# Kernel optimization log

Hardware: AMD Instinct MI355X
Metric: run time of the kernel (lower is better)

## Reference

```python
import jax, jax.numpy as jnp
import numpy as np
from jax import lax

B0, H0, W0, C0 = 16, 32, 32, 512
D_ = C0 // 4      # per-group channels = d_inner (expand=1)
S = 1             # d_state
R = 8             # dt_rank = ceil(D_/16)


def layernorm(x, w, b, eps=1e-5):
    m = jnp.mean(x, axis=-1, keepdims=True)
    v = jnp.mean((x - m) ** 2, axis=-1, keepdims=True)
    return (x - m) / jnp.sqrt(v + eps) * w + b


def silu(x):
    return x * jax.nn.sigmoid(x)


def selective_scan(u, delta, A, Bs, Cs, Dp):
    # u,delta:(B,d,L)  A:(d,S)  Bs,Cs:(B,S,L)  Dp:(d,)
    a = jnp.exp(jnp.einsum('bdl,ds->bdsl', delta, A))      # decay per step
    bx = jnp.einsum('bdl,bsl,bdl->bdsl', delta, Bs, u)     # input injection
    def comb(c1, c2):
        a1, b1 = c1
        a2, b2 = c2
        return (a1 * a2, a2 * b1 + b2)
    _, h = lax.associative_scan(comb, (a, bx), axis=-1)    # h_t = a_t h_{t-1} + b_t
    return jnp.einsum('bdsl,bsl->bdl', h, Cs) + Dp[None, :, None] * u


def ss2d(xg, direction, ipw, cw, cb, xpw, dtw, dtb, Alog, Dp, onw, onb, opw):
    # xg: (B,H,W,dm); single-direction SS2D branch (CrossScan_i / CrossMerge_i)
    Bsz, Hh, Ww, dm = xg.shape
    xz = jnp.einsum('bhwc,oc->bhwo', xg, ipw)              # in_proj -> 2*d_inner
    xc, z = jnp.split(xz, 2, axis=-1)
    xc = xc.transpose(0, 3, 1, 2)                           # (B,d,H,W)
    xc = lax.conv_general_dilated(xc, cw, (1, 1), [(1, 1), (1, 1)],
                                  dimension_numbers=('NCHW', 'OIHW', 'NCHW'),
                                  feature_group_count=dm) + cb[None, :, None, None]
    xc = silu(xc)
    L = Hh * Ww
    if direction == 0:
        xs = xc.reshape(Bsz, dm, L)                         # row-major forward
    elif direction == 1:
        xs = xc.transpose(0, 1, 3, 2).reshape(Bsz, dm, L)   # column-major forward
    elif direction == 2:
        xs = xc.reshape(Bsz, dm, L)[:, :, ::-1]             # row-major reversed
    else:
        xs = xc.transpose(0, 1, 3, 2).reshape(Bsz, dm, L)[:, :, ::-1]
    xd = jnp.einsum('bdl,cd->bcl', xs, xpw)                 # x_proj -> (dt,B,C)
    dts, Bc, Cc = jnp.split(xd, [R, R + S], axis=1)
    delta = jax.nn.softplus(jnp.einsum('brl,dr->bdl', dts, dtw) + dtb[None, :, None])
    A = -jnp.exp(Alog)                                      # (d,S)
    y = selective_scan(xs, delta, A, Bc, Cc, Dp)
    if direction == 0:
        yhw = y.reshape(Bsz, dm, Hh, Ww)
    elif direction == 1:
        yhw = y.reshape(Bsz, dm, Ww, Hh).transpose(0, 1, 3, 2)
    elif direction == 2:
        yhw = y[:, :, ::-1].reshape(Bsz, dm, Hh, Ww)
    else:
        yhw = y[:, :, ::-1].reshape(Bsz, dm, Ww, Hh).transpose(0, 1, 3, 2)
    yo = yhw.transpose(0, 2, 3, 1)                          # (B,H,W,d)
    yo = layernorm(yo, onw, onb)
    yo = yo * silu(z)
    return jnp.einsum('bhwd,od->bhwo', yo, opw)             # out_proj


def setup_inputs() -> dict:
    key = jax.random.key(0)
    ks = jax.random.split(key, 12)
    def rn(k, shape, scale=0.02):
        return (jax.random.normal(k, shape) * scale).astype(jnp.float32)
    return dict(
        x=jax.random.normal(ks[0], (B0, H0 * W0, C0), dtype=jnp.float32),
        H=H0, W=W0,
        norm_w=jnp.ones((C0,), jnp.float32), norm_b=jnp.zeros((C0,), jnp.float32),
        fc_w=rn(ks[1], (C0, C0)), fc_b=jnp.zeros((C0,), jnp.float32),
        eca_w=rn(ks[2], (3,), 0.3),
        skip_scale=jnp.ones((), jnp.float32),
        proj_w=rn(ks[3], (C0, C0)), proj_b=jnp.zeros((C0,), jnp.float32),
        in_proj_w=rn(ks[4], (4, 2 * D_, D_)),
        conv_w=rn(ks[5], (4, D_, 1, 3, 3), 0.1), conv_b=jnp.zeros((4, D_), jnp.float32),
        x_proj_w=rn(ks[6], (4, R + 2 * S, D_)),
        dt_proj_w=rn(ks[7], (4, D_, R), 0.1), dt_proj_b=rn(ks[8], (4, D_), 0.1),
        A_log=jnp.zeros((4, D_, S), jnp.float32),           # A = -1 (d_state=1 init)
        D_param=jnp.ones((4, D_), jnp.float32),
        out_norm_w=jnp.ones((4, D_), jnp.float32), out_norm_b=jnp.zeros((4, D_), jnp.float32),
        out_proj_w=rn(ks[9], (4, D_, D_)),
    )


def reference(x, H, W, norm_w, norm_b, fc_w, fc_b, eca_w, skip_scale, proj_w, proj_b,
              in_proj_w, conv_w, conv_b, x_proj_w, dt_proj_w, dt_proj_b, A_log, D_param,
              out_norm_w, out_norm_b, out_proj_w):
    Bsz, N, Cc = x.shape
    xn = layernorm(x, norm_w, norm_b)
    # ECA-style channel gate: mean over tokens, 1D conv (k=3) over channel axis
    z_avg = jnp.mean(xn, axis=1)                            # (B,C)
    zp = jnp.pad(z_avg, ((0, 0), (1, 1)))
    y_eca = eca_w[0] * zp[:, :-2] + eca_w[1] * zp[:, 1:-1] + eca_w[2] * zp[:, 2:]
    gate = jax.nn.sigmoid(jnp.einsum('bc,oc->bo', z_avg, fc_w) + fc_b + y_eca)
    xh = xn.reshape(Bsz, H, W, Cc)
    groups = jnp.split(xh, 4, axis=-1)
    ys = []
    for g in range(4):                                      # 4 directional SS2D branches
        ys.append(ss2d(groups[g], g, in_proj_w[g], conv_w[g], conv_b[g], x_proj_w[g],
                       dt_proj_w[g], dt_proj_b[g], A_log[g], D_param[g],
                       out_norm_w[g], out_norm_b[g], out_proj_w[g]))
    xm = jnp.concatenate(ys, axis=-1) * skip_scale * xh
    xm = xm.reshape(Bsz, N, Cc) * gate[:, None, :]
    xm = layernorm(xm, norm_w, norm_b)
    return jnp.einsum('bnc,oc->bno', xm, proj_w) + proj_b
```

## Files before the change

### kernel.cpp

```cpp
#include <hip/hip_runtime.h>
#include <math.h>

#define NTOK 16384
#define NC 512
#define ND 128
#define NCH 64
#define CST 16

typedef __attribute__((ext_vector_type(8))) short bf16x8;
typedef __attribute__((ext_vector_type(4))) float f32x4;

#define LOG2E 1.4426950408889634f
#define LN2   0.6931471805599453f

__device__ __forceinline__ float fexp(float x){ return __builtin_amdgcn_exp2f(x * LOG2E); }
__device__ __forceinline__ float flog(float x){ return __builtin_amdgcn_logf(x) * LN2; }
__device__ __forceinline__ float sigf(float x){ return 1.f/(1.f + fexp(-x)); }

__device__ __forceinline__ float b2f(ushort u){ unsigned x = ((unsigned)u)<<16; return __builtin_bit_cast(float,x); }
__device__ __forceinline__ ushort f2b(float f){
  unsigned u = __builtin_bit_cast(unsigned,f);
  u += 0x7fff + ((u>>16)&1);
  return (ushort)(u>>16);
}

__device__ __forceinline__ int perm_pos(int g, int l){
  switch(g){
    case 0: return l;
    case 1: return ((l & 31) << 5) | (l >> 5);
    case 2: return 1023 - l;
    default:{ int ll = 1023 - l; return ((ll & 31) << 5) | (ll >> 5); }
  }
}

__device__ __forceinline__ void gload16(const void* g, void* l){
  __builtin_amdgcn_global_load_lds((const __attribute__((address_space(1))) void*)g,
                                   (__attribute__((address_space(3))) void*)l, 16, 0, 0);
}

__global__ __launch_bounds__(256) void k_tobf16_4(
    const float* __restrict__ s1, int n1, ushort* __restrict__ d1,
    const float* __restrict__ s2, int n2, ushort* __restrict__ d2,
    const float* __restrict__ s3, int n3, ushort* __restrict__ d3,
    const float* __restrict__ s4, int n4, ushort* __restrict__ d4){
  int i = blockIdx.x*256 + threadIdx.x;
  if (i < n1) d1[i] = f2b(s1[i]);
  else if (i < n1+n2) d2[i-n1] = f2b(s2[i-n1]);
  else if (i < n1+n2+n3) d3[i-n1-n2] = f2b(s3[i-n1-n2]);
  else if (i < n1+n2+n3+n4) d4[i-n1-n2-n3] = f2b(s4[i-n1-n2-n3]);
}

__global__ __launch_bounds__(256) void k_ln512(const float* __restrict__ x,
    const float* __restrict__ w, const float* __restrict__ b, ushort* __restrict__ out){
  int wv = threadIdx.x >> 6, lane = threadIdx.x & 63;
  int t = blockIdx.x*4 + wv;
  const float* xr = x + (size_t)t*NC + lane*8;
  float4 a = *(const float4*)xr;
  float4 c = *(const float4*)(xr+4);
  float e[8] = {a.x,a.y,a.z,a.w,c.x,c.y,c.z,c.w};
  float s = 0.f, sq = 0.f;
  #pragma unroll
  for (int i=0;i<8;i++){ s += e[i]; sq += e[i]*e[i]; }
  #pragma unroll
  for (int o=1;o<64;o<<=1){ s += __shfl_xor(s,o); sq += __shfl_xor(sq,o); }
  float m = s*(1.f/NC);
  float var = sq*(1.f/NC) - m*m;
  float rs = rsqrtf(var + 1e-5f);
  const float4* wr = (const float4*)(w + lane*8);
  const float4* br = (const float4*)(b + lane*8);
  float4 w0 = wr[0], w1 = wr[1], b0 = br[0], b1 = br[1];
  float wv8[8] = {w0.x,w0.y,w0.z,w0.w,w1.x,w1.y,w1.z,w1.w};
  float bv8[8] = {b0.x,b0.y,b0.z,b0.w,b1.x,b1.y,b1.z,b1.w};
  bf16x8 o8;
  #pragma unroll
  for (int i=0;i<8;i++) ((ushort*)&o8)[i] = f2b((e[i]-m)*rs*wv8[i]+bv8[i]);
  *(bf16x8*)(out + (size_t)t*NC + lane*8) = o8;
}

__global__ __launch_bounds__(512) void k_cm1(const ushort* __restrict__ xn,
    float* __restrict__ part){
  int c = threadIdx.x;
  const ushort* base = xn + ((size_t)blockIdx.x*32)*NC + c;
  float acc = 0.f;
  for (int n=0;n<32;n++) acc += b2f(base[(size_t)n*NC]);
  part[(size_t)blockIdx.x*NC + c] = acc;
}
__global__ __launch_bounds__(512) void k_cm2(const float* __restrict__ part,
    float* __restrict__ zavg){
  int b = blockIdx.x, c = threadIdx.x;
  float acc = 0.f;
  for (int i=0;i<32;i++) acc += part[(size_t)(b*32+i)*NC + c];
  zavg[b*NC+c] = acc * (1.f/1024.f);
}

__global__ __launch_bounds__(256) void k_gate(const float* __restrict__ zavg,
    const float* __restrict__ fcw, const float* __restrict__ fcb,
    const float* __restrict__ ew, float* __restrict__ gate){
  __shared__ float za[NC];
  int b = blockIdx.x >> 7, og = blockIdx.x & 127;
  int tid = threadIdx.x, lane = tid & 63, wv = tid >> 6;
  za[tid]     = zavg[b*NC + tid];
  za[tid+256] = zavg[b*NC + tid + 256];
  __syncthreads();
  int o = og*4 + wv;
  const float* wr = fcw + (size_t)o*NC;
  float acc = 0.f;
  #pragma unroll
  for (int i=0;i<8;i++) acc += za[lane + i*64]*wr[lane + i*64];
  #pragma unroll
  for (int off=1;off<64;off<<=1) acc += __shfl_xor(acc, off);
  if (lane==0){
    float left  = (o>0)    ? za[o-1] : 0.f;
    float right = (o<NC-1) ? za[o+1] : 0.f;
    float ye = ew[0]*left + ew[1]*za[o] + ew[2]*right;
    gate[b*NC+o] = sigf(acc + fcb[o] + ye);
  }
}

__global__ __launch_bounds__(256) void k_gemm_bf16(
    const ushort* __restrict__ A, int lda, long sAz,
    const ushort* __restrict__ Bw, int ldb, long sBz, int K,
    ushort* __restrict__ C0, int ldc0, ushort* __restrict__ C1, int ldc1,
    int nsplit, long sCz,
    float* __restrict__ Cf, int ldcf, const float* __restrict__ bias)
{
  __shared__ __align__(16) ushort Asm[128*64];
  __shared__ __align__(16) ushort Bsm[128*64];
  const int z = blockIdx.z;
  A  += (size_t)z*sAz;
  Bw += (size_t)z*sBz;
  if (C0) C0 += (size_t)z*sCz;
  if (C1) C1 += (size_t)z*sCz;
  const int tid = threadIdx.x;
  const int lane = tid & 63, wid = tid >> 6;
  const int wm = wid >> 1, wn = wid & 1;
  const int m0 = blockIdx.y * 128, n0 = blockIdx.x * 128;

  const ushort* ga[4]; const ushort* gb[4]; int ldst[4];
  #pragma unroll
  for (int j=0;j<4;j++){
    int c = tid + 256*j;
    int r = c >> 3;
    int kb = ((c & 7) << 4) ^ ((r & 7) << 4);
    ga[j] = A  + (size_t)(m0 + r)*lda + (kb >> 1);
    gb[j] = Bw + (size_t)(n0 + r)*ldb + (kb >> 1);
    ldst[j] = c * 8;
  }

  f32x4 acc[4][4];
  #pragma unroll
  for (int i=0;i<4;i++)
    #pragma unroll
    for (int j=0;j<4;j++) acc[i][j] = (f32x4){0.f,0.f,0.f,0.f};

  const int lc = lane & 15;
  const int kgrp = (lane >> 4) << 4;

  for (int k0 = 0; k0 < K; k0 += 64){
    #pragma unroll
    for (int j=0;j<4;j++) gload16(ga[j] + k0, Asm + ldst[j]);
    #pragma unroll
    for (int j=0;j<4;j++) gload16(gb[j] + k0, Bsm + ldst[j]);
    __syncthreads();
    #pragma unroll
    for (int kk=0; kk<2; kk++){
      bf16x8 af[4], bfr[4];
      #pragma unroll
      for (int i=0;i<4;i++){
        int ra = wm*64 + i*16 + lc;
        int kb = kk*64 + kgrp;
        af[i] = *(const bf16x8*)((const char*)Asm + ra*128 + (kb ^ ((ra&7)<<4)));
        int rb = wn*64 + i*16 + lc;
        bfr[i] = *(const bf16x8*)((const char*)Bsm + rb*128 + (kb ^ ((rb&7)<<4)));
      }
      #pragma unroll
      for (int i=0;i<4;i++)
        #pragma unroll
        for (int j=0;j<4;j++)
          acc[i][j] = __builtin_amdgcn_mfma_f32_16x16x32_bf16(af[i], bfr[j], acc[i][j], 0, 0, 0);
    }
    __syncthreads();
  }

  const int lr = (lane >> 4) * 4;
  if (Cf){
    #pragma unroll
    for (int i=0;i<4;i++)
      #pragma unroll
      for (int j=0;j<4;j++){
        int row = m0 + wm*64 + i*16 + lr;
        int col = n0 + wn*64 + j*16 + lc;
        float bv = bias ? bias[col] : 0.f;
        #pragma unroll
        for (int r=0;r<4;r++)
          Cf[(size_t)(row+r)*ldcf + col] = acc[i][j][r] + bv;
      }
  } else {
    #pragma unroll
    for (int i=0;i<4;i++)
      #pragma unroll
      for (int j=0;j<4;j++){
        int row = m0 + wm*64 + i*16 + lr;
        int col = n0 + wn*64 + j*16 + lc;
        #pragma unroll
        for (int r=0;r<4;r++){
          ushort hv = f2b(acc[i][j][r]);
          if (col < nsplit) C0[(size_t)(row+r)*ldc0 + col] = hv;
          else              C1[(size_t)(row+r)*ldc1 + col - nsplit] = hv;
        }
      }
  }
}

__global__ __launch_bounds__(256) void k_convxp(const ushort* __restrict__ xc,
    const float* __restrict__ cw, const float* __restrict__ cb,
    const ushort* __restrict__ xpw_b, ushort* __restrict__ u, float* __restrict__ xd){
  __shared__ __align__(16) ushort xin[4*32*128];
  __shared__ __align__(16) ushort su[64][136];
  int g = blockIdx.z, tid = threadIdx.x;
  int blk = blockIdx.x;
  int bimg = blk >> 4, rp = blk & 15;
  int t0 = blk * 64;
  const ushort* xcg = xc + (size_t)g*NTOK*ND;

  #pragma unroll
  for (int j=0;j<8;j++){
    int c = tid + 256*j;
    int r = c >> 9;
    int rest = c & 511;
    int gr = 2*rp + r - 1;
    gr = min(max(gr, 0), 31);
    int w = rest >> 4, p = rest & 15;
    gload16(xcg + ((size_t)((bimg<<10) | (gr<<5) | w))*ND + p*8, (ushort*)xin + c*8);
  }

  int p = tid & 15, d0 = p*8;
  float w_[9][8]; float bias[8];
  {
    const float* wk = cw + (size_t)(g*ND + d0)*9;
    #pragma unroll
    for (int j=0;j<8;j++)
      #pragma unroll
      for (int k9=0;k9<9;k9++) w_[k9][j] = wk[j*9+k9];
    const float* cbp = cb + g*ND + d0;
    #pragma unroll
    for (int j=0;j<8;j++) bias[j] = cbp[j];
  }
  __syncthreads();

  #pragma unroll
  for (int pass=0; pass<4; pass++){
    int lt = pass*16 + (tid>>4);
    int hl = lt >> 5, w = lt & 31;
    int t = t0 + lt;
    float acc[8];
    #pragma unroll
    for (int j=0;j<8;j++) acc[j] = bias[j];
    #pragma unroll
    for (int kh=0;kh<3;kh++){
      int gr = 2*rp + hl + kh - 1;
      if (gr < 0 || gr >= 32) continue;
      #pragma unroll
      for (int kw=0;kw<3;kw++){
        int w2 = w + kw - 1;
        if (w2 < 0 || w2 >= 32) continue;
        bf16x8 v = *(const bf16x8*)&xin[((hl+kh)*32 + w2)*128 + d0];
        #pragma unroll
        for (int j=0;j<8;j++) acc[j] = fmaf(b2f(((ushort*)&v)[j]), w_[kh*3+kw][j], acc[j]);
      }
    }
    bf16x8 o8;
    #pragma unroll
    for (int j=0;j<8;j++){
      float uv = acc[j] * sigf(acc[j]);
      ((ushort*)&o8)[j] = f2b(uv);
    }
    *(bf16x8*)(u + ((size_t)g*NTOK + t)*ND + d0) = o8;
    *(bf16x8*)&su[lt][d0] = o8;
  }
  __syncthreads();

  int lane = tid & 63, wv = tid >> 6;
  int c = lane & 15;
  int kg = (lane >> 4) * 8;
  int cc = c < 10 ? c : 0;
  f32x4 acc4 = (f32x4){0.f,0.f,0.f,0.f};
  #pragma unroll
  for (int ks=0; ks<4; ks++){
    bf16x8 af = *(const bf16x8*)&su[wv*16 + (lane & 15)][ks*32 + kg];
    bf16x8 bfv = *(const bf16x8*)(xpw_b + (size_t)(g*10+cc)*128 + ks*32 + kg);
    if (c >= 10) bfv = (bf16x8){0,0,0,0,0,0,0,0};
    acc4 = __builtin_amdgcn_mfma_f32_16x16x32_bf16(af, bfv, acc4, 0, 0, 0);
  }
  if (c < 10){
    #pragma unroll
    for (int r=0;r<4;r++){
      int row = (lane >> 4)*4 + r;
      int t = t0 + wv*16 + row;
      xd[((size_t)g*NTOK + t)*12 + c] = acc4[r];
    }
  }
}

struct ScanCtx {
  float Ad, dtb_d;
  float w[8];
};

__device__ __forceinline__ void scan_step(const ScanCtx& c, float uv,
    const float4& x0, const float4& x1, float Bv,
    float& h, float& ap){
  float a = c.dtb_d;
  a = fmaf(x0.x, c.w[0], a); a = fmaf(x0.y, c.w[1], a);
  a = fmaf(x0.z, c.w[2], a); a = fmaf(x0.w, c.w[3], a);
  a = fmaf(x1.x, c.w[4], a); a = fmaf(x1.y, c.w[5], a);
  a = fmaf(x1.z, c.w[6], a); a = fmaf(x1.w, c.w[7], a);
  float dl = (a > 15.f) ? a : flog(1.f + fexp(a));
  float av = fexp(dl * c.Ad);
  h = fmaf(av, h, dl*Bv*uv);
  ap *= av;
}

__global__ __launch_bounds__(128) void k_scan1(const ushort* __restrict__ u,
    const float* __restrict__ xd, const float* __restrict__ Alog,
    const float* __restrict__ dtw, const float* __restrict__ dtb,
    float* __restrict__ chA, float* __restrict__ chB){
  int d = threadIdx.x, g = blockIdx.z;
  int b = blockIdx.x >> 6, ch = blockIdx.x & 63;
  ScanCtx c;
  c.Ad = -fexp(Alog[g*ND+d]);
  c.dtb_d = dtb[g*ND+d];
  const float4* wr = (const float4*)(dtw + (size_t)(g*ND+d)*8);
  float4 w0 = wr[0], w1 = wr[1];
  c.w[0]=w0.x;c.w[1]=w0.y;c.w[2]=w0.z;c.w[3]=w0.w;
  c.w[4]=w1.x;c.w[5]=w1.y;c.w[6]=w1.z;c.w[7]=w1.w;
  float h = 0.f, ap = 1.f;
  int l0 = ch*CST;
  #pragma unroll 4
  for (int s=0;s<CST;s++){
    int pp = perm_pos(g, l0 + s);
    size_t base = (size_t)g*NTOK + ((b<<10)|pp);
    float uv = b2f(u[base*ND + d]);
    const float4* xr = (const float4*)(xd + base*12);
    float4 x0 = xr[0], x1 = xr[1], x2 = xr[2];
    scan_step(c, uv, x0, x1, x2.x, h, ap);
  }
  size_t o = (((size_t)g*16 + b)*NCH + ch)*ND + d;
  chA[o]=ap; chB[o]=h;
}

__global__ __launch_bounds__(128) void k_scomb(const float* __restrict__ chA,
    const float* __restrict__ chB, float* __restrict__ hIn){
  int b = blockIdx.x, g = blockIdx.z, d = threadIdx.x;
  size_t base = (((size_t)g*16 + b)*NCH)*ND + d;
  float hrun = 0.f;
  #pragma unroll
  for (int ch=0; ch<NCH; ch++){
    size_t o = base + (size_t)ch*ND;
    float a = chA[o], bb = chB[o];
    hIn[o] = hrun;
    hrun = fmaf(a, hrun, bb);
  }
}

__global__ __launch_bounds__(128) void k_scan3(const ushort* __restrict__ u,
    const float* __restrict__ xd, const float* __restrict__ Alog,
    const float* __restrict__ dtw, const float* __restrict__ dtb,
    const float* __restrict__ Dp, const float* __restrict__ hIn,
    ushort* __restrict__ y){
  int d = threadIdx.x, g = blockIdx.z;
  int b = blockIdx.x >> 6, ch = blockIdx.x & 63;
  ScanCtx c;
  c.Ad = -fexp(Alog[g*ND+d]);
  c.dtb_d = dtb[g*ND+d];
  float Dd = Dp[g*ND+d];
  const float4* wr = (const float4*)(dtw + (size_t)(g*ND+d)*8);
  float4 w0 = wr[0], w1 = wr[1];
  c.w[0]=w0.x;c.w[1]=w0.y;c.w[2]=w0.z;c.w[3]=w0.w;
  c.w[4]=w1.x;c.w[5]=w1.y;c.w[6]=w1.z;c.w[7]=w1.w;
  float h = hIn[(((size_t)g*16 + b)*NCH + ch)*ND + d];
  float ap = 1.f;
  int l0 = ch*CST;
  #pragma unroll 4
  for (int s=0;s<CST;s++){
    int pp = perm_pos(g, l0 + s);
    size_t base = (size_t)g*NTOK + ((b<<10)|pp);
    float uv = b2f(u[base*ND + d]);
    const float4* xr = (const float4*)(xd + base*12);
    float4 x0 = xr[0], x1 = xr[1], x2 = xr[2];
    scan_step(c, uv, x0, x1, x2.x, h, ap);
    y[base*ND + d] = f2b(fmaf(h, x2.y, Dd*uv));
  }
}

__global__ __launch_bounds__(256) void k_yo(const ushort* __restrict__ y,
    const ushort* __restrict__ zg, const float* __restrict__ onw,
    const float* __restrict__ onb, ushort* __restrict__ yo){
  int tid = threadIdx.x, g = blockIdx.z;
  int lt = tid >> 4, p = tid & 15;
  int t = blockIdx.x*16 + lt;
  size_t base = ((size_t)g*NTOK + t)*ND + p*8;
  bf16x8 yv8 = *(const bf16x8*)(y + base);
  float e[8];
  float s = 0.f, sq = 0.f;
  #pragma unroll
  for (int i=0;i<8;i++){
    e[i] = b2f(((ushort*)&yv8)[i]);
    s += e[i]; sq += e[i]*e[i];
  }
  #pragma unroll
  for (int o=1;o<16;o<<=1){ s += __shfl_xor(s,o); sq += __shfl_xor(sq,o); }
  float m = s*(1.f/ND);
  float var = sq*(1.f/ND) - m*m;
  float rs = rsqrtf(var + 1e-5f);
  const float4* wr = (const float4*)(onw + g*ND + p*8);
  const float4* br = (const float4*)(onb + g*ND + p*8);
  float4 w0 = wr[0], w1 = wr[1], b0 = br[0], b1 = br[1];
  float wv8[8] = {w0.x,w0.y,w0.z,w0.w,w1.x,w1.y,w1.z,w1.w};
  float bv8[8] = {b0.x,b0.y,b0.z,b0.w,b1.x,b1.y,b1.z,b1.w};
  bf16x8 zv = *(const bf16x8*)(zg + base);
  bf16x8 o8;
  #pragma unroll
  for (int i=0;i<8;i++){
    float yn = (e[i]-m)*rs*wv8[i]+bv8[i];
    float z = b2f(((ushort*)&zv)[i]);
    ((ushort*)&o8)[i] = f2b(yn * z * sigf(z));
  }
  *(bf16x8*)(yo + base) = o8;
}

__global__ __launch_bounds__(256) void k_gateln(const ushort* __restrict__ ybuf,
    const ushort* __restrict__ xn, const float* __restrict__ gate,
    const float* __restrict__ skip, const float* __restrict__ w,
    const float* __restrict__ b, ushort* __restrict__ out){
  int wv = threadIdx.x >> 6, lane = threadIdx.x & 63;
  int t = blockIdx.x*4 + wv, bb = t >> 10;
  float ss = skip[0];
  size_t o0 = (size_t)t*NC + lane*8;
  bf16x8 yv = *(const bf16x8*)(ybuf + o0);
  bf16x8 xv = *(const bf16x8*)(xn + o0);
  const float4* gr = (const float4*)(gate + bb*NC + lane*8);
  float4 g0 = gr[0], g1 = gr[1];
  float gv8[8] = {g0.x,g0.y,g0.z,g0.w,g1.x,g1.y,g1.z,g1.w};
  float e[8];
  float s = 0.f, sq = 0.f;
  #pragma unroll
  for (int i=0;i<8;i++){
    e[i] = b2f(((ushort*)&yv)[i]) * ss * b2f(((ushort*)&xv)[i]) * gv8[i];
    s += e[i]; sq += e[i]*e[i];
  }
  #pragma unroll
  for (int o=1;o<64;o<<=1){ s += __shfl_xor(s,o); sq += __shfl_xor(sq,o); }
  float m = s*(1.f/NC);
  float var = sq*(1.f/NC) - m*m;
  float rs = rsqrtf(var + 1e-5f);
  const float4* wr = (const float4*)(w + lane*8);
  const float4* br = (const float4*)(b + lane*8);
  float4 w0 = wr[0], w1 = wr[1], b0 = br[0], b1 = br[1];
  float wv8[8] = {w0.x,w0.y,w0.z,w0.w,w1.x,w1.y,w1.z,w1.w};
  float bv8[8] = {b0.x,b0.y,b0.z,b0.w,b1.x,b1.y,b1.z,b1.w};
  bf16x8 o8;
  #pragma unroll
  for (int i=0;i<8;i++) ((ushort*)&o8)[i] = f2b((e[i]-m)*rs*wv8[i]+bv8[i]);
  *(bf16x8*)(out + o0) = o8;
}

extern "C" void kernel_launch(void* const* d_in, const int* in_sizes, int n_in,
                              void* d_out, int out_size, void* d_ws, size_t ws_size,
                              hipStream_t stream) {
  const float* x          = (const float*)d_in[0];
  const float* norm_w     = (const float*)d_in[3];
  const float* norm_b     = (const float*)d_in[4];
  const float* fc_w       = (const float*)d_in[5];
  const float* fc_b       = (const float*)d_in[6];
  const float* eca_w      = (const float*)d_in[7];
  const float* skip_scale = (const float*)d_in[8];
  const float* proj_w     = (const float*)d_in[9];
  const float* proj_b     = (const float*)d_in[10];
  const float* in_proj_w  = (const float*)d_in[11];
  const float* conv_w     = (const float*)d_in[12];
  const float* conv_b     = (const float*)d_in[13];
  const float* x_proj_w   = (const float*)d_in[14];
  const float* dt_proj_w  = (const float*)d_in[15];
  const float* dt_proj_b  = (const float*)d_in[16];
  const float* A_log      = (const float*)d_in[17];
  const float* D_param    = (const float*)d_in[18];
  const float* out_norm_w = (const float*)d_in[19];
  const float* out_norm_b = (const float*)d_in[20];
  const float* out_proj_w = (const float*)d_in[21];
  float* out = (float*)d_out;
  float* ws  = (float*)d_ws;

  ushort* xn_b   = (ushort*)(ws);
  ushort* ybuf_b = (ushort*)(ws + 4194304);
  ushort* xc4    = (ushort*)(ws + 8388608);
  ushort* zg4    = (ushort*)(ws + 12582912);
  ushort* yo4    = (ushort*)(ws + 16777216);
  ushort* u4b    = (ushort*)(ws + 20971520);
  ushort* y4b    = (ushort*)(ws + 25165824);
  float*  xd4    = ws + 29360128;
  float*  chA    = ws + 30146560;
  float*  chB    = ws + 30670848;
  float*  hIn    = ws + 31195136;
  float*  zavg   = ws + 31719424;
  float*  gatep  = ws + 31727616;
  float*  part   = ws + 31735808;
  ushort* wb_in  = (ushort*)(ws + 31997952);
  ushort* wb_out = (ushort*)(ws + 32063488);
  ushort* wb_prj = (ushort*)(ws + 32096256);
  ushort* wb_xp  = (ushort*)(ws + 32227328);
  ushort* xmn_b  = (ushort*)(ws + 32229888);

  k_ln512<<<dim3(NTOK/4), dim3(256), 0, stream>>>(x, norm_w, norm_b, xn_b);
  k_cm1<<<dim3(512), dim3(512), 0, stream>>>(xn_b, part);
  k_cm2<<<dim3(16), dim3(512), 0, stream>>>(part, zavg);
  k_gate<<<dim3(16*128), dim3(256), 0, stream>>>(zavg, fc_w, fc_b, eca_w, gatep);
  k_tobf16_4<<<dim3(1812), dim3(256), 0, stream>>>(
      in_proj_w, 131072, wb_in, out_proj_w, 65536, wb_out,
      proj_w, 262144, wb_prj, x_proj_w, 5120, wb_xp);

  k_gemm_bf16<<<dim3(2,128,4), dim3(256), 0, stream>>>(
      xn_b, NC, 128, wb_in, 128, 256*128, 128,
      xc4, 128, zg4, 128, 128, (long)NTOK*128,
      (float*)nullptr, 0, (const float*)nullptr);

  k_convxp<<<dim3(NTOK/64,1,4), dim3(256), 0, stream>>>(
      xc4, conv_w, conv_b, wb_xp, u4b, xd4);

  k_scan1<<<dim3(16*NCH,1,4), dim3(128), 0, stream>>>(
      u4b, xd4, A_log, dt_proj_w, dt_proj_b, chA, chB);
  k_scomb<<<dim3(16,1,4), dim3(128), 0, stream>>>(chA, chB, hIn);
  k_scan3<<<dim3(16*NCH,1,4), dim3(128), 0, stream>>>(
      u4b, xd4, A_log, dt_proj_w, dt_proj_b, D_param, hIn, y4b);

  k_yo<<<dim3(NTOK/16,1,4), dim3(256), 0, stream>>>(
      y4b, zg4, out_norm_w, out_norm_b, yo4);

  k_gemm_bf16<<<dim3(1,128,4), dim3(256), 0, stream>>>(
      yo4, 128, (long)NTOK*128, wb_out, 128, 128*128, 128,
      ybuf_b, NC, ybuf_b, NC, 1<<30, 128,
      (float*)nullptr, 0, (const float*)nullptr);

  k_gateln<<<dim3(NTOK/4), dim3(256), 0, stream>>>(
      ybuf_b, xn_b, gatep, skip_scale, norm_w, norm_b, xmn_b);

  k_gemm_bf16<<<dim3(4,128,1), dim3(256), 0, stream>>>(
      xmn_b, NC, 0, wb_prj, NC, 0, NC,
      (ushort*)nullptr, 0, (ushort*)nullptr, 0, 0, 0,
      out, NC, proj_b);
}
```

Before: 136.3 us.

## Widen GEMM N-tile, fold scan combine into scan3, batch gate, vectorize channel mean

The GEMM is templated so one block computes two 128-wide N tiles and reuses the A tile across both, halving A reloads for in_proj and the final projection. The separate chunk-combine kernel is removed, and each scan3 block instead recomputes its incoming state serially from the chunk summaries. The gate kernel now handles all 16 batches per block with the weights kept in registers, and the channel-mean kernel uses vectorized 16-byte loads with an LDS reduction. The trade-offs are fewer GEMM blocks (lower occupancy, more accumulator registers) and redundant serial prefix work in scan3 that grows with chunk index.

```diff
diff --git a/kernel.cpp b/kernel.cpp
--- a/kernel.cpp
+++ b/kernel.cpp
@@ -77,46 +77,72 @@
   *(bf16x8*)(out + (size_t)t*NC + lane*8) = o8;
 }
 
-__global__ __launch_bounds__(512) void k_cm1(const ushort* __restrict__ xn,
+__global__ __launch_bounds__(256) void k_cm1(const ushort* __restrict__ xn,
     float* __restrict__ part){
-  int c = threadIdx.x;
-  const ushort* base = xn + ((size_t)blockIdx.x*32)*NC + c;
-  float acc = 0.f;
-  for (int n=0;n<32;n++) acc += b2f(base[(size_t)n*NC]);
-  part[(size_t)blockIdx.x*NC + c] = acc;
+  __shared__ float pl[3][512];
+  int tid = threadIdx.x, rs = tid >> 6, l8 = (tid & 63)*8;
+  const ushort* base = xn + ((size_t)blockIdx.x*64 + rs*16)*NC + l8;
+  float a[8] = {0,0,0,0,0,0,0,0};
+  #pragma unroll
+  for (int it=0; it<16; it++){
+    bf16x8 v = *(const bf16x8*)(base + (size_t)it*NC);
+    #pragma unroll
+    for (int j=0;j<8;j++) a[j] += b2f(((ushort*)&v)[j]);
+  }
+  if (rs > 0){
+    #pragma unroll
+    for (int j=0;j<8;j++) pl[rs-1][l8+j] = a[j];
+  }
+  __syncthreads();
+  if (rs == 0){
+    #pragma unroll
+    for (int j=0;j<8;j++)
+      part[(size_t)blockIdx.x*512 + l8 + j] = a[j] + pl[0][l8+j] + pl[1][l8+j] + pl[2][l8+j];
+  }
 }
 __global__ __launch_bounds__(512) void k_cm2(const float* __restrict__ part,
     float* __restrict__ zavg){
   int b = blockIdx.x, c = threadIdx.x;
   float acc = 0.f;
-  for (int i=0;i<32;i++) acc += part[(size_t)(b*32+i)*NC + c];
+  for (int i=0;i<16;i++) acc += part[(size_t)(b*16+i)*512 + c];
   zavg[b*NC+c] = acc * (1.f/1024.f);
 }
 
 __global__ __launch_bounds__(256) void k_gate(const float* __restrict__ zavg,
     const float* __restrict__ fcw, const float* __restrict__ fcb,
     const float* __restrict__ ew, float* __restrict__ gate){
-  __shared__ float za[NC];
-  int b = blockIdx.x >> 7, og = blockIdx.x & 127;
+  __shared__ float za[16][512];
+  int og = blockIdx.x;
   int tid = threadIdx.x, lane = tid & 63, wv = tid >> 6;
-  za[tid]     = zavg[b*NC + tid];
-  za[tid+256] = zavg[b*NC + tid + 256];
+  #pragma unroll
+  for (int i=0;i<32;i++){
+    int idx = tid + i*256;
+    za[idx >> 9][idx & 511] = zavg[idx];
+  }
   __syncthreads();
   int o = og*4 + wv;
+  float wreg[8];
   const float* wr = fcw + (size_t)o*NC;
-  float acc = 0.f;
-  #pragma unroll
-  for (int i=0;i<8;i++) acc += za[lane + i*64]*wr[lane + i*64];
-  #pragma unroll
-  for (int off=1;off<64;off<<=1) acc += __shfl_xor(acc, off);
-  if (lane==0){
-    float left  = (o>0)    ? za[o-1] : 0.f;
-    float right = (o<NC-1) ? za[o+1] : 0.f;
-    float ye = ew[0]*left + ew[1]*za[o] + ew[2]*right;
-    gate[b*NC+o] = sigf(acc + fcb[o] + ye);
-  }
-}
-
+  #pragma unroll
+  for (int i=0;i<8;i++) wreg[i] = wr[lane + i*64];
+  float e0 = ew[0], e1 = ew[1], e2 = ew[2];
+  float fb = fcb[o];
+  for (int b=0;b<16;b++){
+    float acc = 0.f;
+    #pragma unroll
+    for (int i=0;i<8;i++) acc += za[b][lane + i*64]*wreg[i];
+    #pragma unroll
+    for (int off=1;off<64;off<<=1) acc += __shfl_xor(acc, off);
+    if (lane==0){
+      float left  = (o>0)    ? za[b][o-1] : 0.f;
+      float right = (o<NC-1) ? za[b][o+1] : 0.f;
+      float ye = e0*left + e1*za[b][o] + e2*right;
+      gate[b*NC+o] = sigf(acc + fb + ye);
+    }
+  }
+}
+
+template<int NT>
 __global__ __launch_bounds__(256) void k_gemm_bf16(
     const ushort* __restrict__ A, int lda, long sAz,
     const ushort* __restrict__ Bw, int ldb, long sBz, int K,
@@ -125,7 +151,7 @@
     float* __restrict__ Cf, int ldcf, const float* __restrict__ bias)
 {
   __shared__ __align__(16) ushort Asm[128*64];
-  __shared__ __align__(16) ushort Bsm[128*64];
+  __shared__ __align__(16) ushort Bsm[NT*128*64];
   const int z = blockIdx.z;
   A  += (size_t)z*sAz;
   Bw += (size_t)z*sBz;
@@ -134,24 +160,28 @@
   const int tid = threadIdx.x;
   const int lane = tid & 63, wid = tid >> 6;
   const int wm = wid >> 1, wn = wid & 1;
-  const int m0 = blockIdx.y * 128, n0 = blockIdx.x * 128;
-
-  const ushort* ga[4]; const ushort* gb[4]; int ldst[4];
+  const int m0 = blockIdx.y * 128, n0 = blockIdx.x * (NT*128);
+
+  const ushort* ga[4]; const ushort* gb[NT][4]; int ldst[4];
   #pragma unroll
   for (int j=0;j<4;j++){
     int c = tid + 256*j;
     int r = c >> 3;
     int kb = ((c & 7) << 4) ^ ((r & 7) << 4);
-    ga[j] = A  + (size_t)(m0 + r)*lda + (kb >> 1);
-    gb[j] = Bw + (size_t)(n0 + r)*ldb + (kb >> 1);
+    ga[j] = A + (size_t)(m0 + r)*lda + (kb >> 1);
+    #pragma unroll
+    for (int nt=0;nt<NT;nt++)
+      gb[nt][j] = Bw + (size_t)(n0 + nt*128 + r)*ldb + (kb >> 1);
     ldst[j] = c * 8;
   }
 
-  f32x4 acc[4][4];
-  #pragma unroll
-  for (int i=0;i<4;i++)
-    #pragma unroll
-    for (int j=0;j<4;j++) acc[i][j] = (f32x4){0.f,0.f,0.f,0.f};
+  f32x4 acc[NT][4][4];
+  #pragma unroll
+  for (int nt=0;nt<NT;nt++)
+    #pragma unroll
+    for (int i=0;i<4;i++)
+      #pragma unroll
+      for (int j=0;j<4;j++) acc[nt][i][j] = (f32x4){0.f,0.f,0.f,0.f};
 
   const int lc = lane & 15;
   const int kgrp = (lane >> 4) << 4;
@@ -160,55 +190,68 @@
     #pragma unroll
     for (int j=0;j<4;j++) gload16(ga[j] + k0, Asm + ldst[j]);
     #pragma unroll
-    for (int j=0;j<4;j++) gload16(gb[j] + k0, Bsm + ldst[j]);
+    for (int nt=0;nt<NT;nt++)
+      #pragma unroll
+      for (int j=0;j<4;j++) gload16(gb[nt][j] + k0, Bsm + nt*8192 + ldst[j]);
     __syncthreads();
     #pragma unroll
     for (int kk=0; kk<2; kk++){
-      bf16x8 af[4], bfr[4];
+      bf16x8 af[4];
       #pragma unroll
       for (int i=0;i<4;i++){
         int ra = wm*64 + i*16 + lc;
         int kb = kk*64 + kgrp;
         af[i] = *(const bf16x8*)((const char*)Asm + ra*128 + (kb ^ ((ra&7)<<4)));
-        int rb = wn*64 + i*16 + lc;
-        bfr[i] = *(const bf16x8*)((const char*)Bsm + rb*128 + (kb ^ ((rb&7)<<4)));
       }
+      #pragma unroll
+      for (int nt=0;nt<NT;nt++){
+        bf16x8 bfr[4];
+        #pragma unroll
+        for (int i=0;i<4;i++){
+          int rb = wn*64 + i*16 + lc;
+          int kb = kk*64 + kgrp;
+          bfr[i] = *(const bf16x8*)((const char*)Bsm + nt*16384 + rb*128 + (kb ^ ((rb&7)<<4)));
+        }
+        #pragma unroll
+        for (int i=0;i<4;i++)
+          #pragma unroll
+          for (int j=0;j<4;j++)
+            acc[nt][i][j] = __builtin_amdgcn_mfma_f32_16x16x32_bf16(af[i], bfr[j], acc[nt][i][j], 0, 0, 0);
+      }
+    }
+    __syncthreads();
+  }
+
+  const int lr = (lane >> 4) * 4;
+  #pragma unroll
+  for (int nt=0;nt<NT;nt++){
+    if (Cf){
       #pragma unroll
       for (int i=0;i<4;i++)
         #pragma unroll
-        for (int j=0;j<4;j++)
-          acc[i][j] = __builtin_amdgcn_mfma_f32_16x16x32_bf16(af[i], bfr[j], acc[i][j], 0, 0, 0);
+        for (int j=0;j<4;j++){
+          int row = m0 + wm*64 + i*16 + lr;
+          int col = n0 + nt*128 + wn*64 + j*16 + lc;
+          float bv = bias ? bias[col] : 0.f;
+          #pragma unroll
+          for (int r=0;r<4;r++)
+            Cf[(size_t)(row+r)*ldcf + col] = acc[nt][i][j][r] + bv;
+        }
+    } else {
+      #pragma unroll
+      for (int i=0;i<4;i++)
+        #pragma unroll
+        for (int j=0;j<4;j++){
+          int row = m0 + wm*64 + i*16 + lr;
+          int col = n0 + nt*128 + wn*64 + j*16 + lc;
+          #pragma unroll
+          for (int r=0;r<4;r++){
+            ushort hv = f2b(acc[nt][i][j][r]);
+            if (col < nsplit) C0[(size_t)(row+r)*ldc0 + col] = hv;
+            else              C1[(size_t)(row+r)*ldc1 + col - nsplit] = hv;
+          }
+        }
     }
-    __syncthreads();
-  }
-
-  const int lr = (lane >> 4) * 4;
-  if (Cf){
-    #pragma unroll
-    for (int i=0;i<4;i++)
-      #pragma unroll
-      for (int j=0;j<4;j++){
-        int row = m0 + wm*64 + i*16 + lr;
-        int col = n0 + wn*64 + j*16 + lc;
-        float bv = bias ? bias[col] : 0.f;
-        #pragma unroll
-        for (int r=0;r<4;r++)
-          Cf[(size_t)(row+r)*ldcf + col] = acc[i][j][r] + bv;
-      }
-  } else {
-    #pragma unroll
-    for (int i=0;i<4;i++)
-      #pragma unroll
-      for (int j=0;j<4;j++){
-        int row = m0 + wm*64 + i*16 + lr;
-        int col = n0 + wn*64 + j*16 + lc;
-        #pragma unroll
-        for (int r=0;r<4;r++){
-          ushort hv = f2b(acc[i][j][r]);
-          if (col < nsplit) C0[(size_t)(row+r)*ldc0 + col] = hv;
-          else              C1[(size_t)(row+r)*ldc1 + col - nsplit] = hv;
-        }
-      }
   }
 }
 
@@ -349,25 +392,11 @@
   chA[o]=ap; chB[o]=h;
 }
 
-__global__ __launch_bounds__(128) void k_scomb(const float* __restrict__ chA,
-    const float* __restrict__ chB, float* __restrict__ hIn){
-  int b = blockIdx.x, g = blockIdx.z, d = threadIdx.x;
-  size_t base = (((size_t)g*16 + b)*NCH)*ND + d;
-  float hrun = 0.f;
-  #pragma unroll
-  for (int ch=0; ch<NCH; ch++){
-    size_t o = base + (size_t)ch*ND;
-    float a = chA[o], bb = chB[o];
-    hIn[o] = hrun;
-    hrun = fmaf(a, hrun, bb);
-  }
-}
-
 __global__ __launch_bounds__(128) void k_scan3(const ushort* __restrict__ u,
     const float* __restrict__ xd, const float* __restrict__ Alog,
     const float* __restrict__ dtw, const float* __restrict__ dtb,
-    const float* __restrict__ Dp, const float* __restrict__ hIn,
-    ushort* __restrict__ y){
+    const float* __restrict__ Dp, const float* __restrict__ chA,
+    const float* __restrict__ chB, ushort* __restrict__ y){
   int d = threadIdx.x, g = blockIdx.z;
   int b = blockIdx.x >> 6, ch = blockIdx.x & 63;
   ScanCtx c;
@@ -378,7 +407,12 @@
   float4 w0 = wr[0], w1 = wr[1];
   c.w[0]=w0.x;c.w[1]=w0.y;c.w[2]=w0.z;c.w[3]=w0.w;
   c.w[4]=w1.x;c.w[5]=w1.y;c.w[6]=w1.z;c.w[7]=w1.w;
-  float h = hIn[(((size_t)g*16 + b)*NCH + ch)*ND + d];
+  size_t cbase = (((size_t)g*16 + b)*NCH)*ND + d;
+  float h = 0.f;
+  for (int k=0;k<ch;k++){
+    size_t o = cbase + (size_t)k*ND;
+    h = fmaf(chA[o], h, chB[o]);
+  }
   float ap = 1.f;
   int l0 = ch*CST;
   #pragma unroll 4
@@ -501,7 +535,6 @@
   float*  xd4    = ws + 29360128;
   float*  chA    = ws + 30146560;
   float*  chB    = ws + 30670848;
-  float*  hIn    = ws + 31195136;
   float*  zavg   = ws + 31719424;
   float*  gatep  = ws + 31727616;
   float*  part   = ws + 31735808;
@@ -512,14 +545,14 @@
   ushort* xmn_b  = (ushort*)(ws + 32229888);
 
   k_ln512<<<dim3(NTOK/4), dim3(256), 0, stream>>>(x, norm_w, norm_b, xn_b);
-  k_cm1<<<dim3(512), dim3(512), 0, stream>>>(xn_b, part);
+  k_cm1<<<dim3(256), dim3(256), 0, stream>>>(xn_b, part);
   k_cm2<<<dim3(16), dim3(512), 0, stream>>>(part, zavg);
-  k_gate<<<dim3(16*128), dim3(256), 0, stream>>>(zavg, fc_w, fc_b, eca_w, gatep);
+  k_gate<<<dim3(128), dim3(256), 0, stream>>>(zavg, fc_w, fc_b, eca_w, gatep);
   k_tobf16_4<<<dim3(1812), dim3(256), 0, stream>>>(
       in_proj_w, 131072, wb_in, out_proj_w, 65536, wb_out,
       proj_w, 262144, wb_prj, x_proj_w, 5120, wb_xp);
 
-  k_gemm_bf16<<<dim3(2,128,4), dim3(256), 0, stream>>>(
+  k_gemm_bf16<2><<<dim3(1,128,4), dim3(256), 0, stream>>>(
       xn_b, NC, 128, wb_in, 128, 256*128, 128,
       xc4, 128, zg4, 128, 128, (long)NTOK*128,
       (float*)nullptr, 0, (const float*)nullptr);
@@ -529,14 +562,13 @@
 
   k_scan1<<<dim3(16*NCH,1,4), dim3(128), 0, stream>>>(
       u4b, xd4, A_log, dt_proj_w, dt_proj_b, chA, chB);
-  k_scomb<<<dim3(16,1,4), dim3(128), 0, stream>>>(chA, chB, hIn);
   k_scan3<<<dim3(16*NCH,1,4), dim3(128), 0, stream>>>(
-      u4b, xd4, A_log, dt_proj_w, dt_proj_b, D_param, hIn, y4b);
+      u4b, xd4, A_log, dt_proj_w, dt_proj_b, D_param, chA, chB, y4b);
 
   k_yo<<<dim3(NTOK/16,1,4), dim3(256), 0, stream>>>(
       y4b, zg4, out_norm_w, out_norm_b, yo4);
 
-  k_gemm_bf16<<<dim3(1,128,4), dim3(256), 0, stream>>>(
+  k_gemm_bf16<1><<<dim3(1,128,4), dim3(256), 0, stream>>>(
       yo4, 128, (long)NTOK*128, wb_out, 128, 128*128, 128,
       ybuf_b, NC, ybuf_b, NC, 1<<30, 128,
       (float*)nullptr, 0, (const float*)nullptr);
@@ -544,7 +576,7 @@
   k_gateln<<<dim3(NTOK/4), dim3(256), 0, stream>>>(
       ybuf_b, xn_b, gatep, skip_scale, norm_w, norm_b, xmn_b);
 
-  k_gemm_bf16<<<dim3(4,128,1), dim3(256), 0, stream>>>(
+  k_gemm_bf16<2><<<dim3(2,128,1), dim3(256), 0, stream>>>(
       xmn_b, NC, 0, wb_prj, NC, 0, NC,
       (ushort*)nullptr, 0, (ushort*)nullptr, 0, 0, 0,
       out, NC, proj_b);
```

Result: slower. 170.7 us (+25.2%).
